# Kernel optimization log

Measured on AMD Instinct MI355X. Metric: run time of the kernel, lower is better.

## Reference

```python
import jax, jax.numpy as jnp
import numpy as np

B, L, E, MODES = 32, 2048, 512, 32  # batch, seq_len, d_model, kept Fourier modes (mode_select='low')


def setup_inputs() -> dict:
    key = jax.random.key(0)
    ks = jax.random.split(key, 6)
    scale = 1.0 / (E * E)  # FourierBlock scale = 1/(in_channels*out_channels), torch.rand init
    lin = E ** -0.5
    return {
        "queries": jax.random.normal(ks[0], (B, L, E), jnp.float32),
        "Wq": jax.random.normal(ks[1], (E, E), jnp.float32) * lin,
        "bq": jnp.zeros((E,), jnp.float32),
        "W1r": jax.random.uniform(ks[2], (E, E, MODES), jnp.float32) * scale,
        "W1i": jax.random.uniform(ks[3], (E, E, MODES), jnp.float32) * scale,
        "Wo": jax.random.normal(ks[4], (E, E), jnp.float32) * lin,
        "bo": jnp.zeros((E,), jnp.float32),
    }


def reference(queries, Wq, bq, W1r, W1i, Wo, bo):
    Bn, Ln, En = queries.shape
    # query projection
    q = queries @ Wq.T + bq                                    # (B, L, E)
    # FourierBlock: FFT along time, keep low `MODES` bins, complex channel mixing, inverse FFT
    xf = jnp.fft.rfft(q, axis=1)                               # (B, L//2+1, E) complex64
    W1 = (W1r + 1j * W1i).astype(jnp.complex64)                # (E_in, E_out, M)
    sel = xf[:, :MODES, :]                                     # (B, M, E) selected modes (mode_select='low')
    out_sel = jnp.einsum('bmi,iom->bmo', sel, W1)              # per-mode complex E x E mixing
    nfreq = Ln // 2 + 1
    out_ft = jnp.zeros((Bn, nfreq, En), jnp.complex64).at[:, :MODES, :].set(out_sel)
    x = jnp.fft.irfft(out_ft, n=Ln, axis=1)                    # (B, L, E) real
    # output projection (attn is None in the original; return the tensor output)
    return x @ Wo.T + bo
```

## Files before the change

kernel.cpp:

```cpp
#include <hip/hip_runtime.h>
#include <hip/hip_bf16.h>

typedef _Float16 f16;
typedef _Float16 f16x8 __attribute__((ext_vector_type(8)));
typedef _Float16 f16x4 __attribute__((ext_vector_type(4)));
typedef float f32x4 __attribute__((ext_vector_type(4)));

#define PADK 40
#define PADK2 72

#define W1SCALE 262144.0f
#define W1DESCALE 3.814697265625e-06f

static __device__ __forceinline__ f32x4 mfma16(f16x8 a, f16x8 b, f32x4 c) {
  return __builtin_amdgcn_mfma_f32_16x16x32_f16(a, b, c, 0, 0, 0);
}

__global__ __launch_bounds__(256) void k_tables(f16* __restrict__ FhT, f16* __restrict__ Gh) {
  int idx = blockIdx.x * 256 + threadIdx.x;
  const float w = 6.28318530717958647692f / 2048.0f;
  {
    int k2 = idx >> 11, l = idx & 2047;
    int k = k2 & 31;
    float th = (float)((k * l) & 2047) * w;
    float v = (k2 < 32) ? cosf(th) : -sinf(th);
    FhT[k2 * 2048 + l] = (f16)v;
  }
  {
    int l = idx >> 6, kk = idx & 63;
    int k = kk & 31;
    float th = (float)((k * l) & 2047) * w;
    float v;
    if (kk < 32) v = ((k == 0) ? 1.0f : 2.0f) * (1.0f / 2048.0f) * cosf(th);
    else         v = (k == 0) ? 0.0f : (-2.0f / 2048.0f) * sinf(th);
    Gh[l * 64 + kk] = (f16)v;
  }
}

__global__ __launch_bounds__(256) void k_cast_f16(const float* __restrict__ src,
                                                  f16* __restrict__ dst, int n4) {
  int i = blockIdx.x * 256 + threadIdx.x;
  if (i < n4) {
    float4 v = ((const float4*)src)[i];
    f16x4 o = {(f16)v.x, (f16)v.y, (f16)v.z, (f16)v.w};
    *(f16x4*)(dst + (size_t)i * 4) = o;
  }
}

__global__ __launch_bounds__(256) void k_w1t2(const float* __restrict__ W1r,
                                              const float* __restrict__ W1i,
                                              f16* __restrict__ W1rT,
                                              f16* __restrict__ W1iT) {
  __shared__ __align__(16) f16 WL[256 * 72];
  const int o0 = blockIdx.x * 8, i0 = blockIdx.y * 64;
  const int t = threadIdx.x;
  for (int pass = 0; pass < 2; ++pass) {
    const float* src = pass ? W1i : W1r;
    f16* dst = pass ? W1iT : W1rT;
    __syncthreads();
#pragma unroll
    for (int j = 0; j < 16; ++j) {
      int idx = t + 256 * j;
      int mq = idx & 7, oo = (idx >> 3) & 7, ii = idx >> 6;
      const float4 v = *(const float4*)(src + (size_t)(i0 + ii) * 16384 + (o0 + oo) * 32 + mq * 4);
      WL[(oo * 32 + mq * 4 + 0) * 72 + ii] = (f16)(W1SCALE * v.x);
      WL[(oo * 32 + mq * 4 + 1) * 72 + ii] = (f16)(W1SCALE * v.y);
      WL[(oo * 32 + mq * 4 + 2) * 72 + ii] = (f16)(W1SCALE * v.z);
      WL[(oo * 32 + mq * 4 + 3) * 72 + ii] = (f16)(W1SCALE * v.w);
    }
    __syncthreads();
#pragma unroll
    for (int j = 0; j < 8; ++j) {
      int idx = t + 256 * j;
      int i8 = idx & 7, m = (idx >> 3) & 31, oo = idx >> 8;
      f16x8 v = *(const f16x8*)(&WL[(oo * 32 + m) * 72 + i8 * 8]);
      *(f16x8*)(dst + (size_t)m * 262144 + (size_t)(o0 + oo) * 512 + i0 + i8 * 8) = v;
    }
  }
}

__global__ __launch_bounds__(256) void k_dft_fwd(const f16* __restrict__ FhT,
                                                 const float* __restrict__ queries,
                                                 float* __restrict__ p32) {
  __shared__ __align__(16) f16 As[64 * PADK];
  __shared__ __align__(16) f16 Bs[64 * PADK];
  const int n0 = blockIdx.x * 64;
  const int b  = blockIdx.y;
  const int kb = blockIdx.z * 256;
  const int t = threadIdx.x;
  const int wid = t >> 6, lane = t & 63;
  const int mh = wid & 1, nh = wid >> 1;
  const int arow = t >> 2, ac8 = (t & 3) << 3;
  const int bcol = t & 63, bkg = t >> 6;
  f32x4 acc[2][2] = {};
  for (int k0 = kb; k0 < kb + 256; k0 += 32) {
    __syncthreads();
    *(f16x8*)(As + arow * PADK + ac8) =
        *(const f16x8*)(FhT + (size_t)arow * 2048 + k0 + ac8);
    const float* qp = queries + ((size_t)b * 2048 + k0 + bkg * 8) * 512 + n0 + bcol;
    float v[8];
#pragma unroll
    for (int r = 0; r < 8; ++r) v[r] = qp[(size_t)r * 512];
    f16x4 lo = {(f16)v[0], (f16)v[1], (f16)v[2], (f16)v[3]};
    f16x4 hi = {(f16)v[4], (f16)v[5], (f16)v[6], (f16)v[7]};
    *(f16x4*)(Bs + bcol * PADK + bkg * 8) = lo;
    *(f16x4*)(Bs + bcol * PADK + bkg * 8 + 4) = hi;
    __syncthreads();
    const int kofs = (lane >> 4) << 3;
    f16x8 a0 = *(const f16x8*)(As + (mh * 32 + 0  + (lane & 15)) * PADK + kofs);
    f16x8 a1 = *(const f16x8*)(As + (mh * 32 + 16 + (lane & 15)) * PADK + kofs);
    f16x8 b0 = *(const f16x8*)(Bs + (nh * 32 + 0  + (lane & 15)) * PADK + kofs);
    f16x8 b1 = *(const f16x8*)(Bs + (nh * 32 + 16 + (lane & 15)) * PADK + kofs);
    acc[0][0] = mfma16(a0, b0, acc[0][0]);
    acc[0][1] = mfma16(a0, b1, acc[0][1]);
    acc[1][0] = mfma16(a1, b0, acc[1][0]);
    acc[1][1] = mfma16(a1, b1, acc[1][1]);
  }
#pragma unroll
  for (int mf = 0; mf < 2; ++mf)
#pragma unroll
    for (int nf = 0; nf < 2; ++nf)
#pragma unroll
      for (int r = 0; r < 4; ++r) {
        int k2 = mh * 32 + mf * 16 + ((lane >> 4) << 2) + r;
        int col = n0 + nh * 32 + nf * 16 + (lane & 15);
        p32[((size_t)blockIdx.z * 2048 + b * 64 + k2) * 512 + col] = acc[mf][nf][r];
      }
}

__global__ __launch_bounds__(256) void k_reduce8(const float* __restrict__ p,
                                                 f16* __restrict__ dst) {
  size_t i4 = (size_t)blockIdx.x * 256 + threadIdx.x;
  float4 s = {0.f, 0.f, 0.f, 0.f};
#pragma unroll
  for (int c = 0; c < 8; ++c) {
    float4 v = ((const float4*)p)[(size_t)c * 262144 + i4];
    s.x += v.x; s.y += v.y; s.z += v.z; s.w += v.w;
  }
  f16x4 o = {(f16)s.x, (f16)s.y, (f16)s.z, (f16)s.w};
  *(f16x4*)(dst + i4 * 4) = o;
}

__global__ __launch_bounds__(256) void k_gemm_nk(const f16* __restrict__ A,
                                                 const f16* __restrict__ Bnk,
                                                 f16* __restrict__ C,
                                                 const float* __restrict__ bias0,
                                                 float bscale) {
  __shared__ __align__(16) f16 As[64 * PADK];
  __shared__ __align__(16) f16 Bs[32 * PADK];
  const int n0 = blockIdx.x * 32, m0 = blockIdx.y * 64;
  const int t = threadIdx.x;
  const int wid = t >> 6, lane = t & 63;
  const int mh = wid & 1, nh = wid >> 1;
  const int row = t >> 2, c8 = (t & 3) << 3;
  f32x4 acc[2] = {};
  for (int k0 = 0; k0 < 512; k0 += 32) {
    __syncthreads();
    *(f16x8*)(As + row * PADK + c8) =
        *(const f16x8*)(A + (size_t)(m0 + row) * 512 + k0 + c8);
    if (t < 128)
      *(f16x8*)(Bs + row * PADK + c8) =
          *(const f16x8*)(Bnk + (size_t)(n0 + row) * 512 + k0 + c8);
    __syncthreads();
    const int kofs = (lane >> 4) << 3;
    f16x8 a0 = *(const f16x8*)(As + (mh * 32 + 0  + (lane & 15)) * PADK + kofs);
    f16x8 a1 = *(const f16x8*)(As + (mh * 32 + 16 + (lane & 15)) * PADK + kofs);
    f16x8 b0 = *(const f16x8*)(Bs + (nh * 16 + (lane & 15)) * PADK + kofs);
    acc[0] = mfma16(a0, b0, acc[0]);
    acc[1] = mfma16(a1, b0, acc[1]);
  }
#pragma unroll
  for (int mf = 0; mf < 2; ++mf)
#pragma unroll
    for (int r = 0; r < 4; ++r) {
      int mg = m0 + mh * 32 + mf * 16 + ((lane >> 4) << 2) + r;
      int col = n0 + nh * 16 + (lane & 15);
      float cv = acc[mf][r];
      if (bias0 != nullptr && (mg & 63) == 0) cv += bscale * bias0[col];
      C[(size_t)mg * 512 + col] = (f16)cv;
    }
}

__global__ __launch_bounds__(256) void k_modes(const f16* __restrict__ sel,
                                               const f16* __restrict__ W1rT,
                                               const f16* __restrict__ W1iT,
                                               f16* __restrict__ osel) {
  __shared__ __align__(16) f16 ARs[32 * PADK];
  __shared__ __align__(16) f16 AIs[32 * PADK];
  __shared__ __align__(16) f16 BRs[32 * PADK];
  __shared__ __align__(16) f16 BIs[32 * PADK];
  const int n0 = blockIdx.x * 32, m = blockIdx.y;
  const int t = threadIdx.x, wid = t >> 6, lane = t & 63;
  const int mh = wid & 1, nh = wid >> 1;
  const f16* Wr = W1rT + (size_t)m * 262144;
  const f16* Wi = W1iT + (size_t)m * 262144;
  const int srow = lane >> 1, sc0 = (lane & 1) << 3;
  f32x4 accR, accI;
#pragma unroll
  for (int r = 0; r < 4; ++r) { accR[r] = 0.f; accI[r] = 0.f; }
  for (int k0 = 0; k0 < 512; k0 += 32) {
    __syncthreads();
    if (wid == 0) {
      *(f16x8*)(ARs + srow * PADK + sc0) =
          *(const f16x8*)(sel + ((size_t)srow * 64 + m) * 512 + k0 + sc0);
      *(f16x8*)(ARs + srow * PADK + sc0 + 16) =
          *(const f16x8*)(sel + ((size_t)srow * 64 + m) * 512 + k0 + sc0 + 16);
    } else if (wid == 1) {
      *(f16x8*)(AIs + srow * PADK + sc0) =
          *(const f16x8*)(sel + ((size_t)srow * 64 + 32 + m) * 512 + k0 + sc0);
      *(f16x8*)(AIs + srow * PADK + sc0 + 16) =
          *(const f16x8*)(sel + ((size_t)srow * 64 + 32 + m) * 512 + k0 + sc0 + 16);
    } else if (wid == 2) {
      *(f16x8*)(BRs + srow * PADK + sc0) =
          *(const f16x8*)(Wr + (size_t)(n0 + srow) * 512 + k0 + sc0);
      *(f16x8*)(BRs + srow * PADK + sc0 + 16) =
          *(const f16x8*)(Wr + (size_t)(n0 + srow) * 512 + k0 + sc0 + 16);
    } else {
      *(f16x8*)(BIs + srow * PADK + sc0) =
          *(const f16x8*)(Wi + (size_t)(n0 + srow) * 512 + k0 + sc0);
      *(f16x8*)(BIs + srow * PADK + sc0 + 16) =
          *(const f16x8*)(Wi + (size_t)(n0 + srow) * 512 + k0 + sc0 + 16);
    }
    __syncthreads();
    const int kofs = (lane >> 4) << 3;
    f16x8 ar = *(const f16x8*)(ARs + (mh * 16 + (lane & 15)) * PADK + kofs);
    f16x8 ai = *(const f16x8*)(AIs + (mh * 16 + (lane & 15)) * PADK + kofs);
    f16x8 ain = -ai;
    f16x8 br = *(const f16x8*)(BRs + (nh * 16 + (lane & 15)) * PADK + kofs);
    f16x8 bi = *(const f16x8*)(BIs + (nh * 16 + (lane & 15)) * PADK + kofs);
    accR = mfma16(ar, br, accR);
    accR = mfma16(ain, bi, accR);
    accI = mfma16(ar, bi, accI);
    accI = mfma16(ai, br, accI);
  }
#pragma unroll
  for (int r = 0; r < 4; ++r) {
    int bb = mh * 16 + ((lane >> 4) << 2) + r;
    int col = n0 + nh * 16 + (lane & 15);
    osel[((size_t)bb * 64 + m) * 512 + col] = (f16)accR[r];
    osel[((size_t)bb * 64 + 32 + m) * 512 + col] = (f16)accI[r];
  }
}

__global__ __launch_bounds__(256) void k_dft_inv(const f16* __restrict__ Gh,
                                                 const f16* __restrict__ u,
                                                 const float* __restrict__ bo,
                                                 float* __restrict__ out) {
  __shared__ __align__(16) f16 As[64 * PADK2];
  __shared__ __align__(16) f16 Bs[64 * PADK2];
  const int n0 = blockIdx.x * 64, l0 = blockIdx.y * 64, b = blockIdx.z;
  const int t = threadIdx.x, wid = t >> 6, lane = t & 63;
  const int mh = wid & 1, nh = wid >> 1;
#pragma unroll
  for (int p = 0; p < 2; ++p) {
    int v = t + 256 * p, row = v >> 3, c8 = (v & 7) << 3;
    *(f16x8*)(As + row * PADK2 + c8) = *(const f16x8*)(Gh + (size_t)(l0 + row) * 64 + c8);
  }
  {
    int col = t & 63, kg = t >> 6;
    const f16* up = u + ((size_t)b * 64 + kg * 16) * 512 + n0 + col;
    f16 vv[16];
#pragma unroll
    for (int s = 0; s < 16; ++s) vv[s] = up[(size_t)s * 512];
#pragma unroll
    for (int s4 = 0; s4 < 4; ++s4) {
      f16x4 pk = {vv[s4 * 4], vv[s4 * 4 + 1], vv[s4 * 4 + 2], vv[s4 * 4 + 3]};
      *(f16x4*)(Bs + col * PADK2 + kg * 16 + s4 * 4) = pk;
    }
  }
  __syncthreads();
  f32x4 acc[2][2] = {};
#pragma unroll
  for (int ks = 0; ks < 2; ++ks) {
    const int kofs = ks * 32 + ((lane >> 4) << 3);
    f16x8 a0 = *(const f16x8*)(As + (mh * 32 + 0  + (lane & 15)) * PADK2 + kofs);
    f16x8 a1 = *(const f16x8*)(As + (mh * 32 + 16 + (lane & 15)) * PADK2 + kofs);
    f16x8 b0 = *(const f16x8*)(Bs + (nh * 32 + 0  + (lane & 15)) * PADK2 + kofs);
    f16x8 b1 = *(const f16x8*)(Bs + (nh * 32 + 16 + (lane & 15)) * PADK2 + kofs);
    acc[0][0] = mfma16(a0, b0, acc[0][0]);
    acc[0][1] = mfma16(a0, b1, acc[0][1]);
    acc[1][0] = mfma16(a1, b0, acc[1][0]);
    acc[1][1] = mfma16(a1, b1, acc[1][1]);
  }
#pragma unroll
  for (int mf = 0; mf < 2; ++mf)
#pragma unroll
    for (int nf = 0; nf < 2; ++nf)
#pragma unroll
      for (int r = 0; r < 4; ++r) {
        int l = l0 + mh * 32 + mf * 16 + ((lane >> 4) << 2) + r;
        int col = n0 + nh * 32 + nf * 16 + (lane & 15);
        float cv = acc[mf][nf][r] * W1DESCALE + bo[col];
        out[((size_t)b * 2048 + l) * 512 + col] = cv;
      }
}

extern "C" void kernel_launch(void* const* d_in, const int* in_sizes, int n_in,
                              void* d_out, int out_size, void* d_ws, size_t ws_size,
                              hipStream_t stream) {
  const float* queries = (const float*)d_in[0];
  const float* Wq      = (const float*)d_in[1];
  const float* bq      = (const float*)d_in[2];
  const float* W1r     = (const float*)d_in[3];
  const float* W1i     = (const float*)d_in[4];
  const float* Wo      = (const float*)d_in[5];
  const float* bo      = (const float*)d_in[6];
  float* out           = (float*)d_out;

  char* ws = (char*)d_ws;
  size_t off = 0;
  auto alloc = [&](size_t bytes) {
    off = (off + 255) & ~(size_t)255;
    char* p = ws + off;
    off += bytes;
    return p;
  };
  f16* FhT   = (f16*)alloc((size_t)64 * 2048 * 2);
  f16* Gh    = (f16*)alloc((size_t)2048 * 64 * 2);
  f16* Wq16  = (f16*)alloc((size_t)512 * 512 * 2);
  f16* Wo16  = (f16*)alloc((size_t)512 * 512 * 2);
  f16* W1rT  = (f16*)alloc((size_t)32 * 512 * 512 * 2);
  f16* W1iT  = (f16*)alloc((size_t)32 * 512 * 512 * 2);
  f16* t16   = (f16*)alloc((size_t)2048 * 512 * 2);
  f16* sel   = (f16*)alloc((size_t)2048 * 512 * 2);
  f16* osel  = (f16*)alloc((size_t)2048 * 512 * 2);
  f16* u16   = (f16*)alloc((size_t)2048 * 512 * 2);
  float* p32 = (float*)alloc((size_t)8 * 2048 * 512 * 4);

  hipLaunchKernelGGL(k_tables, dim3(512), dim3(256), 0, stream, FhT, Gh);
  hipLaunchKernelGGL(k_cast_f16, dim3(256), dim3(256), 0, stream, Wq, Wq16, 65536);
  hipLaunchKernelGGL(k_cast_f16, dim3(256), dim3(256), 0, stream, Wo, Wo16, 65536);
  hipLaunchKernelGGL(k_w1t2, dim3(64, 8), dim3(256), 0, stream, W1r, W1i, W1rT, W1iT);
  hipLaunchKernelGGL(k_dft_fwd, dim3(8, 32, 8), dim3(256), 0, stream, FhT, queries, p32);
  hipLaunchKernelGGL(k_reduce8, dim3(1024), dim3(256), 0, stream, p32, t16);
  hipLaunchKernelGGL(k_gemm_nk, dim3(16, 32), dim3(256), 0, stream, t16, Wq16, sel, bq, 2048.0f);
  hipLaunchKernelGGL(k_modes, dim3(16, 32), dim3(256), 0, stream, sel, W1rT, W1iT, osel);
  hipLaunchKernelGGL(k_gemm_nk, dim3(16, 32), dim3(256), 0, stream, osel, Wo16, u16,
                     (const float*)nullptr, 0.0f);
  hipLaunchKernelGGL(k_dft_inv, dim3(8, 32, 32), dim3(256), 0, stream, Gh, u16, bo, out);
}
```

Before: 146.6 us.

## Fuse W1 f16 conversion into mode mixing and restructure forward DFT split

```diff
diff --git a/kernel.cpp b/kernel.cpp
--- a/kernel.cpp
+++ b/kernel.cpp
@@ -47,93 +47,35 @@
   }
 }
 
-__global__ __launch_bounds__(256) void k_w1t2(const float* __restrict__ W1r,
-                                              const float* __restrict__ W1i,
-                                              f16* __restrict__ W1rT,
-                                              f16* __restrict__ W1iT) {
-  __shared__ __align__(16) f16 WL[256 * 72];
-  const int o0 = blockIdx.x * 8, i0 = blockIdx.y * 64;
-  const int t = threadIdx.x;
-  for (int pass = 0; pass < 2; ++pass) {
-    const float* src = pass ? W1i : W1r;
-    f16* dst = pass ? W1iT : W1rT;
-    __syncthreads();
-#pragma unroll
-    for (int j = 0; j < 16; ++j) {
-      int idx = t + 256 * j;
-      int mq = idx & 7, oo = (idx >> 3) & 7, ii = idx >> 6;
-      const float4 v = *(const float4*)(src + (size_t)(i0 + ii) * 16384 + (o0 + oo) * 32 + mq * 4);
-      WL[(oo * 32 + mq * 4 + 0) * 72 + ii] = (f16)(W1SCALE * v.x);
-      WL[(oo * 32 + mq * 4 + 1) * 72 + ii] = (f16)(W1SCALE * v.y);
-      WL[(oo * 32 + mq * 4 + 2) * 72 + ii] = (f16)(W1SCALE * v.z);
-      WL[(oo * 32 + mq * 4 + 3) * 72 + ii] = (f16)(W1SCALE * v.w);
-    }
-    __syncthreads();
-#pragma unroll
-    for (int j = 0; j < 8; ++j) {
-      int idx = t + 256 * j;
-      int i8 = idx & 7, m = (idx >> 3) & 31, oo = idx >> 8;
-      f16x8 v = *(const f16x8*)(&WL[(oo * 32 + m) * 72 + i8 * 8]);
-      *(f16x8*)(dst + (size_t)m * 262144 + (size_t)(o0 + oo) * 512 + i0 + i8 * 8) = v;
-    }
-  }
-}
-
 __global__ __launch_bounds__(256) void k_dft_fwd(const f16* __restrict__ FhT,
-                                                 const float* __restrict__ queries,
-                                                 float* __restrict__ p32) {
-  __shared__ __align__(16) f16 As[64 * PADK];
-  __shared__ __align__(16) f16 Bs[64 * PADK];
-  const int n0 = blockIdx.x * 64;
-  const int b  = blockIdx.y;
-  const int kb = blockIdx.z * 256;
-  const int t = threadIdx.x;
-  const int wid = t >> 6, lane = t & 63;
-  const int mh = wid & 1, nh = wid >> 1;
-  const int arow = t >> 2, ac8 = (t & 3) << 3;
-  const int bcol = t & 63, bkg = t >> 6;
-  f32x4 acc[2][2] = {};
-  for (int k0 = kb; k0 < kb + 256; k0 += 32) {
-    __syncthreads();
-    *(f16x8*)(As + arow * PADK + ac8) =
-        *(const f16x8*)(FhT + (size_t)arow * 2048 + k0 + ac8);
-    const float* qp = queries + ((size_t)b * 2048 + k0 + bkg * 8) * 512 + n0 + bcol;
-    float v[8];
-#pragma unroll
-    for (int r = 0; r < 8; ++r) v[r] = qp[(size_t)r * 512];
-    f16x4 lo = {(f16)v[0], (f16)v[1], (f16)v[2], (f16)v[3]};
-    f16x4 hi = {(f16)v[4], (f16)v[5], (f16)v[6], (f16)v[7]};
-    *(f16x4*)(Bs + bcol * PADK + bkg * 8) = lo;
-    *(f16x4*)(Bs + bcol * PADK + bkg * 8 + 4) = hi;
-    __syncthreads();
-    const int kofs = (lane >> 4) << 3;
-    f16x8 a0 = *(const f16x8*)(As + (mh * 32 + 0  + (lane & 15)) * PADK + kofs);
-    f16x8 a1 = *(const f16x8*)(As + (mh * 32 + 16 + (lane & 15)) * PADK + kofs);
-    f16x8 b0 = *(const f16x8*)(Bs + (nh * 32 + 0  + (lane & 15)) * PADK + kofs);
-    f16x8 b1 = *(const f16x8*)(Bs + (nh * 32 + 16 + (lane & 15)) * PADK + kofs);
-    acc[0][0] = mfma16(a0, b0, acc[0][0]);
-    acc[0][1] = mfma16(a0, b1, acc[0][1]);
-    acc[1][0] = mfma16(a1, b0, acc[1][0]);
-    acc[1][1] = mfma16(a1, b1, acc[1][1]);
-  }
-#pragma unroll
-  for (int mf = 0; mf < 2; ++mf)
-#pragma unroll
-    for (int nf = 0; nf < 2; ++nf)
-#pragma unroll
-      for (int r = 0; r < 4; ++r) {
-        int k2 = mh * 32 + mf * 16 + ((lane >> 4) << 2) + r;
-        int col = n0 + nh * 32 + nf * 16 + (lane & 15);
-        p32[((size_t)blockIdx.z * 2048 + b * 64 + k2) * 512 + col] = acc[mf][nf][r];
-      }
-}
-
-__global__ __launch_bounds__(256) void k_reduce8(const float* __restrict__ p,
-                                                 f16* __restrict__ dst) {
+                                                 const float* __restrict__ q,
+                                                 float* __restrict__ tp) {
+  const int nb = blockIdx.x, b = blockIdx.y, is = blockIdx.z;
+  const int t = threadIdx.x, w = t >> 6, lane = t & 63;
+  const int l15 = lane & 15, kq = lane >> 4, kofs = kq << 3;
+  const int n0 = nb * 16;
+  f32x4 acc = {};
+  const int lbase = is * 1024;
+  for (int lc = lbase; lc < lbase + 1024; lc += 32) {
+    f16x8 a = *(const f16x8*)(FhT + (size_t)(w * 16 + l15) * 2048 + lc + kofs);
+    const float* qp = q + ((size_t)b * 2048 + lc + kofs) * 512 + n0 + l15;
+    f16x8 bf;
+#pragma unroll
+    for (int j = 0; j < 8; ++j) bf[j] = (f16)qp[(size_t)j * 512];
+    acc = mfma16(a, bf, acc);
+  }
+#pragma unroll
+  for (int r = 0; r < 4; ++r) {
+    int k2 = w * 16 + kq * 4 + r;
+    tp[((size_t)is * 2048 + b * 64 + k2) * 512 + n0 + l15] = acc[r];
+  }
+}
+
+__global__ __launch_bounds__(256) void k_reduceN(const float* __restrict__ p,
+                                                 f16* __restrict__ dst, int ns) {
   size_t i4 = (size_t)blockIdx.x * 256 + threadIdx.x;
   float4 s = {0.f, 0.f, 0.f, 0.f};
-#pragma unroll
-  for (int c = 0; c < 8; ++c) {
+  for (int c = 0; c < ns; ++c) {
     float4 v = ((const float4*)p)[(size_t)c * 262144 + i4];
     s.x += v.x; s.y += v.y; s.z += v.z; s.w += v.w;
   }
@@ -145,7 +87,7 @@
                                                  const f16* __restrict__ Bnk,
                                                  f16* __restrict__ C,
                                                  const float* __restrict__ bias0,
-                                                 float bscale) {
+                                                 float bscale, int selt) {
   __shared__ __align__(16) f16 As[64 * PADK];
   __shared__ __align__(16) f16 Bs[32 * PADK];
   const int n0 = blockIdx.x * 32, m0 = blockIdx.y * 64;
@@ -177,68 +119,77 @@
       int col = n0 + nh * 16 + (lane & 15);
       float cv = acc[mf][r];
       if (bias0 != nullptr && (mg & 63) == 0) cv += bscale * bias0[col];
-      C[(size_t)mg * 512 + col] = (f16)cv;
-    }
-}
-
-__global__ __launch_bounds__(256) void k_modes(const f16* __restrict__ sel,
-                                               const f16* __restrict__ W1rT,
-                                               const f16* __restrict__ W1iT,
-                                               f16* __restrict__ osel) {
-  __shared__ __align__(16) f16 ARs[32 * PADK];
-  __shared__ __align__(16) f16 AIs[32 * PADK];
-  __shared__ __align__(16) f16 BRs[32 * PADK];
-  __shared__ __align__(16) f16 BIs[32 * PADK];
-  const int n0 = blockIdx.x * 32, m = blockIdx.y;
-  const int t = threadIdx.x, wid = t >> 6, lane = t & 63;
-  const int mh = wid & 1, nh = wid >> 1;
-  const f16* Wr = W1rT + (size_t)m * 262144;
-  const f16* Wi = W1iT + (size_t)m * 262144;
-  const int srow = lane >> 1, sc0 = (lane & 1) << 3;
-  f32x4 accR, accI;
-#pragma unroll
-  for (int r = 0; r < 4; ++r) { accR[r] = 0.f; accI[r] = 0.f; }
-  for (int k0 = 0; k0 < 512; k0 += 32) {
-    __syncthreads();
-    if (wid == 0) {
-      *(f16x8*)(ARs + srow * PADK + sc0) =
-          *(const f16x8*)(sel + ((size_t)srow * 64 + m) * 512 + k0 + sc0);
-      *(f16x8*)(ARs + srow * PADK + sc0 + 16) =
-          *(const f16x8*)(sel + ((size_t)srow * 64 + m) * 512 + k0 + sc0 + 16);
-    } else if (wid == 1) {
-      *(f16x8*)(AIs + srow * PADK + sc0) =
-          *(const f16x8*)(sel + ((size_t)srow * 64 + 32 + m) * 512 + k0 + sc0);
-      *(f16x8*)(AIs + srow * PADK + sc0 + 16) =
-          *(const f16x8*)(sel + ((size_t)srow * 64 + 32 + m) * 512 + k0 + sc0 + 16);
-    } else if (wid == 2) {
-      *(f16x8*)(BRs + srow * PADK + sc0) =
-          *(const f16x8*)(Wr + (size_t)(n0 + srow) * 512 + k0 + sc0);
-      *(f16x8*)(BRs + srow * PADK + sc0 + 16) =
-          *(const f16x8*)(Wr + (size_t)(n0 + srow) * 512 + k0 + sc0 + 16);
-    } else {
-      *(f16x8*)(BIs + srow * PADK + sc0) =
-          *(const f16x8*)(Wi + (size_t)(n0 + srow) * 512 + k0 + sc0);
-      *(f16x8*)(BIs + srow * PADK + sc0 + 16) =
-          *(const f16x8*)(Wi + (size_t)(n0 + srow) * 512 + k0 + sc0 + 16);
-    }
-    __syncthreads();
-    const int kofs = (lane >> 4) << 3;
-    f16x8 ar = *(const f16x8*)(ARs + (mh * 16 + (lane & 15)) * PADK + kofs);
-    f16x8 ai = *(const f16x8*)(AIs + (mh * 16 + (lane & 15)) * PADK + kofs);
-    f16x8 ain = -ai;
-    f16x8 br = *(const f16x8*)(BRs + (nh * 16 + (lane & 15)) * PADK + kofs);
-    f16x8 bi = *(const f16x8*)(BIs + (nh * 16 + (lane & 15)) * PADK + kofs);
-    accR = mfma16(ar, br, accR);
-    accR = mfma16(ain, bi, accR);
-    accI = mfma16(ar, bi, accI);
-    accI = mfma16(ai, br, accI);
-  }
-#pragma unroll
-  for (int r = 0; r < 4; ++r) {
-    int bb = mh * 16 + ((lane >> 4) << 2) + r;
-    int col = n0 + nh * 16 + (lane & 15);
-    osel[((size_t)bb * 64 + m) * 512 + col] = (f16)accR[r];
-    osel[((size_t)bb * 64 + 32 + m) * 512 + col] = (f16)accI[r];
+      size_t didx = selt ? (((size_t)(mg & 63) * 32 + (mg >> 6)) * 512 + col)
+                         : ((size_t)mg * 512 + col);
+      C[didx] = (f16)cv;
+    }
+}
+
+__global__ __launch_bounds__(512) void k_modes_fused(const float* __restrict__ W1r,
+                                                     const float* __restrict__ W1i,
+                                                     const f16* __restrict__ selT,
+                                                     float* __restrict__ pmode) {
+  __shared__ __align__(16) f16 Wst[2][16][648];
+  const int o0 = blockIdx.x * 16, m0 = blockIdx.y * 16, is = blockIdx.z;
+  const int t = threadIdx.x;
+  const int lane = t & 63, wv = t >> 6;
+  const int l15 = lane & 15, kq = lane >> 4, kofs = kq << 3;
+  const int mq = t & 3, p = t >> 2;
+  const int soo = p & 15, sib = p >> 4;
+  f32x4 accR[2][2] = {}, accI[2][2] = {};
+  const int ibase = is * 128;
+  for (int ch = 0; ch < 4; ++ch) {
+    const int i0c = ibase + ch * 32;
+    __syncthreads();
+#pragma unroll
+    for (int ri = 0; ri < 2; ++ri) {
+      const float* src = ri ? W1i : W1r;
+#pragma unroll
+      for (int qq = 0; qq < 4; ++qq) {
+        int ii = sib + 8 * qq;
+        const float4 v = *(const float4*)(src + (size_t)(i0c + ii) * 16384 +
+                                          (o0 + soo) * 32 + m0 + mq * 4);
+        f16* wp = &Wst[ri][mq * 4][soo * 40 + ii];
+        wp[0 * 648] = (f16)(W1SCALE * v.x);
+        wp[1 * 648] = (f16)(W1SCALE * v.y);
+        wp[2 * 648] = (f16)(W1SCALE * v.z);
+        wp[3 * 648] = (f16)(W1SCALE * v.w);
+      }
+    }
+    __syncthreads();
+#pragma unroll
+    for (int ml = 0; ml < 2; ++ml) {
+      const int mloc = 2 * wv + ml;
+      const int mg = m0 + mloc;
+      f16x8 ar0 = *(const f16x8*)(selT + ((size_t)mg * 32 + 0  + l15) * 512 + i0c + kofs);
+      f16x8 ar1 = *(const f16x8*)(selT + ((size_t)mg * 32 + 16 + l15) * 512 + i0c + kofs);
+      f16x8 ai0 = *(const f16x8*)(selT + ((size_t)(32 + mg) * 32 + 0  + l15) * 512 + i0c + kofs);
+      f16x8 ai1 = *(const f16x8*)(selT + ((size_t)(32 + mg) * 32 + 16 + l15) * 512 + i0c + kofs);
+      f16x8 br = *(const f16x8*)(&Wst[0][mloc][l15 * 40 + kofs]);
+      f16x8 bi = *(const f16x8*)(&Wst[1][mloc][l15 * 40 + kofs]);
+      f16x8 ain0 = -ai0, ain1 = -ai1;
+      accR[ml][0] = mfma16(ar0,  br, accR[ml][0]);
+      accR[ml][0] = mfma16(ain0, bi, accR[ml][0]);
+      accI[ml][0] = mfma16(ar0,  bi, accI[ml][0]);
+      accI[ml][0] = mfma16(ai0,  br, accI[ml][0]);
+      accR[ml][1] = mfma16(ar1,  br, accR[ml][1]);
+      accR[ml][1] = mfma16(ain1, bi, accR[ml][1]);
+      accI[ml][1] = mfma16(ar1,  bi, accI[ml][1]);
+      accI[ml][1] = mfma16(ai1,  br, accI[ml][1]);
+    }
+  }
+#pragma unroll
+  for (int ml = 0; ml < 2; ++ml) {
+    const int mg = m0 + 2 * wv + ml;
+#pragma unroll
+    for (int bt = 0; bt < 2; ++bt)
+#pragma unroll
+      for (int r = 0; r < 4; ++r) {
+        int bb = bt * 16 + kq * 4 + r;
+        int og = o0 + l15;
+        pmode[((size_t)is * 2048 + bb * 64 + mg) * 512 + og]      = accR[ml][bt][r];
+        pmode[((size_t)is * 2048 + bb * 64 + 32 + mg) * 512 + og] = accI[ml][bt][r];
+      }
   }
 }
 
@@ -315,27 +266,28 @@
     off += bytes;
     return p;
   };
-  f16* FhT   = (f16*)alloc((size_t)64 * 2048 * 2);
-  f16* Gh    = (f16*)alloc((size_t)2048 * 64 * 2);
-  f16* Wq16  = (f16*)alloc((size_t)512 * 512 * 2);
-  f16* Wo16  = (f16*)alloc((size_t)512 * 512 * 2);
-  f16* W1rT  = (f16*)alloc((size_t)32 * 512 * 512 * 2);
-  f16* W1iT  = (f16*)alloc((size_t)32 * 512 * 512 * 2);
-  f16* t16   = (f16*)alloc((size_t)2048 * 512 * 2);
-  f16* sel   = (f16*)alloc((size_t)2048 * 512 * 2);
-  f16* osel  = (f16*)alloc((size_t)2048 * 512 * 2);
-  f16* u16   = (f16*)alloc((size_t)2048 * 512 * 2);
-  float* p32 = (float*)alloc((size_t)8 * 2048 * 512 * 4);
+  f16* FhT    = (f16*)alloc((size_t)64 * 2048 * 2);
+  f16* Gh     = (f16*)alloc((size_t)2048 * 64 * 2);
+  f16* Wq16   = (f16*)alloc((size_t)512 * 512 * 2);
+  f16* Wo16   = (f16*)alloc((size_t)512 * 512 * 2);
+  float* tp   = (float*)alloc((size_t)2 * 2048 * 512 * 4);
+  f16* t16    = (f16*)alloc((size_t)2048 * 512 * 2);
+  f16* selT   = (f16*)alloc((size_t)2048 * 512 * 2);
+  float* pmode= (float*)alloc((size_t)4 * 2048 * 512 * 4);
+  f16* osel   = (f16*)alloc((size_t)2048 * 512 * 2);
+  f16* u16    = (f16*)alloc((size_t)2048 * 512 * 2);
 
   hipLaunchKernelGGL(k_tables, dim3(512), dim3(256), 0, stream, FhT, Gh);
   hipLaunchKernelGGL(k_cast_f16, dim3(256), dim3(256), 0, stream, Wq, Wq16, 65536);
   hipLaunchKernelGGL(k_cast_f16, dim3(256), dim3(256), 0, stream, Wo, Wo16, 65536);
-  hipLaunchKernelGGL(k_w1t2, dim3(64, 8), dim3(256), 0, stream, W1r, W1i, W1rT, W1iT);
-  hipLaunchKernelGGL(k_dft_fwd, dim3(8, 32, 8), dim3(256), 0, stream, FhT, queries, p32);
-  hipLaunchKernelGGL(k_reduce8, dim3(1024), dim3(256), 0, stream, p32, t16);
-  hipLaunchKernelGGL(k_gemm_nk, dim3(16, 32), dim3(256), 0, stream, t16, Wq16, sel, bq, 2048.0f);
-  hipLaunchKernelGGL(k_modes, dim3(16, 32), dim3(256), 0, stream, sel, W1rT, W1iT, osel);
+  hipLaunchKernelGGL(k_dft_fwd, dim3(32, 32, 2), dim3(256), 0, stream, FhT, queries, tp);
+  hipLaunchKernelGGL(k_reduceN, dim3(1024), dim3(256), 0, stream, tp, t16, 2);
+  hipLaunchKernelGGL(k_gemm_nk, dim3(16, 32), dim3(256), 0, stream, t16, Wq16, selT,
+                     bq, 2048.0f, 1);
+  hipLaunchKernelGGL(k_modes_fused, dim3(32, 2, 4), dim3(512), 0, stream,
+                     W1r, W1i, selT, pmode);
+  hipLaunchKernelGGL(k_reduceN, dim3(1024), dim3(256), 0, stream, pmode, osel, 4);
   hipLaunchKernelGGL(k_gemm_nk, dim3(16, 32), dim3(256), 0, stream, osel, Wo16, u16,
-                     (const float*)nullptr, 0.0f);
+                     (const float*)nullptr, 0.0f, 0);
   hipLaunchKernelGGL(k_dft_inv, dim3(8, 32, 32), dim3(256), 0, stream, Gh, u16, bo, out);
 }
```

Result: slower. 189.2 us (+29.0%).
